# Performance work log

Measured on AMD Instinct MI355X. Metric: run time of the kernel, lower is better.

The kernel has to match this reference:

```python
import jax, jax.numpy as jnp
import numpy as np

B, N, D, H = 4, 256, 256, 8
HD = D // H
DFF = 4 * D
EPS = 1e-5


def setup_inputs() -> dict:
    key = jax.random.key(0)
    ks = jax.random.split(key, 12)
    s = 0.02
    p = lambda k, shape: (jax.random.normal(k, shape, jnp.float32) * s)
    return dict(
        h=jax.random.normal(ks[0], (B, N, D), jnp.float32),
        e=jax.random.normal(ks[1], (B, N, N, D), jnp.float32),
        We=p(ks[2], (D, D)), be=jnp.zeros((D,), jnp.float32),
        Ws=p(ks[3], (D, D)), bs=jnp.zeros((D,), jnp.float32),
        Wd=p(ks[4], (D, D)), bd=jnp.zeros((D,), jnp.float32),
        Wb=p(ks[5], (D, H)), bb=jnp.zeros((H,), jnp.float32),
        ln1_g=jnp.ones((D,), jnp.float32), ln1_b=jnp.zeros((D,), jnp.float32),
        Wqkv=p(ks[6], (D, 3 * D)), bqkv=jnp.zeros((3 * D,), jnp.float32),
        Wo=p(ks[7], (D, D)), bo=jnp.zeros((D,), jnp.float32),
        ln2_g=jnp.ones((D,), jnp.float32), ln2_b=jnp.zeros((D,), jnp.float32),
        W1=p(ks[8], (D, DFF)), b1=jnp.zeros((DFF,), jnp.float32),
        W2=p(ks[9], (DFF, D)), b2=jnp.zeros((D,), jnp.float32),
    )


def _ln(x, g, b):
    m = jnp.mean(x, axis=-1, keepdims=True)
    v = jnp.mean((x - m) ** 2, axis=-1, keepdims=True)
    return (x - m) * jax.lax.rsqrt(v + EPS) * g + b


def reference(h, e, We, be, Ws, bs, Wd, bd, Wb, bb, ln1_g, ln1_b,
              Wqkv, bqkv, Wo, bo, ln2_g, ln2_b, W1, b1, W2, b2):
    # Edge update: broadcast-add of src/dst node projections + ReLU over [B,N,N,D]
    e_new = jax.nn.relu(e @ We + be
                        + (h @ Ws + bs)[:, :, None, :]   # src -> unsqueeze(2)
                        + (h @ Wd + bd)[:, None, :, :])  # dst -> unsqueeze(1)
    # Per-head additive attention bias [B,H,N,N]
    bias = jnp.einsum('bijd,dh->bhij', e_new, Wb) + bb[None, :, None, None]
    # Pre-LN self-attention with additive bias (torch MHA, eval mode)
    x = _ln(h, ln1_g, ln1_b)
    qkv = x @ Wqkv + bqkv
    q, k, v = jnp.split(qkv, 3, axis=-1)
    q = q.reshape(B, N, H, HD)
    k = k.reshape(B, N, H, HD)
    v = v.reshape(B, N, H, HD)
    scores = jnp.einsum('bihd,bjhd->bhij', q, k) / np.float32(np.sqrt(HD)) + bias
    attn = jax.nn.softmax(scores, axis=-1)
    o = jnp.einsum('bhij,bjhd->bihd', attn, v).reshape(B, N, D)
    h1 = h + (o @ Wo + bo)
    # Pre-LN FFN (exact GELU, as torch nn.GELU default)
    y = _ln(h1, ln2_g, ln2_b)
    h2 = h1 + (jax.nn.gelu(y @ W1 + b1, approximate=False) @ W2 + b2)
    return (h2, e_new)
```

## Files before the change

kernel.cpp:

```cpp
#include <hip/hip_runtime.h>
#include <math.h>

#define EPS 1e-5f

typedef __attribute__((ext_vector_type(4))) float floatx4;
typedef __attribute__((ext_vector_type(8))) short shortx8;

__device__ __forceinline__ unsigned short f2bf(float f){
  union { float f; unsigned u; } v; v.f = f;
  unsigned r = v.u + 0x7FFFu + ((v.u >> 16) & 1u);
  return (unsigned short)(r >> 16);
}
__device__ __forceinline__ float bf2f(unsigned short s){
  union { unsigned u; float f; } v; v.u = ((unsigned)s) << 16;
  return v.f;
}

__global__ __launch_bounds__(256) void k_prep(
    const float* __restrict__ We, const float* __restrict__ Ws, const float* __restrict__ Wd,
    const float* __restrict__ Wqkv, const float* __restrict__ Wo, const float* __restrict__ W1,
    const float* __restrict__ W2, const float* __restrict__ Wb,
    unsigned short* __restrict__ WeT, unsigned short* __restrict__ WsT,
    unsigned short* __restrict__ WdT, unsigned short* __restrict__ WqkvT,
    unsigned short* __restrict__ WoT, unsigned short* __restrict__ W1T,
    unsigned short* __restrict__ W2T, unsigned short* __restrict__ WbT16)
{
  const int blk = blockIdx.x, tid = threadIdx.x;
  if (blk == 240){
#pragma unroll
    for (int hh=0; hh<8; hh++) WbT16[hh*256+tid] = f2bf(Wb[tid*8+hh]);
#pragma unroll
    for (int hh=8; hh<16; hh++) WbT16[hh*256+tid] = 0;
    return;
  }
  const float* src; unsigned short* dst; int K, N, t;
  if (blk < 16)      { src=We;   dst=WeT;   K=256;  N=256;  t=blk; }
  else if (blk < 32) { src=Ws;   dst=WsT;   K=256;  N=256;  t=blk-16; }
  else if (blk < 48) { src=Wd;   dst=WdT;   K=256;  N=256;  t=blk-32; }
  else if (blk < 96) { src=Wqkv; dst=WqkvT; K=256;  N=768;  t=blk-48; }
  else if (blk < 112){ src=Wo;   dst=WoT;   K=256;  N=256;  t=blk-96; }
  else if (blk < 176){ src=W1;   dst=W1T;   K=256;  N=1024; t=blk-112; }
  else               { src=W2;   dst=W2T;   K=1024; N=256;  t=blk-176; }
  const int tpr = N >> 6;
  const int k0 = (t / tpr) << 6, n0 = (t % tpr) << 6;
  __shared__ float tile[64][65];
#pragma unroll
  for (int s=0;s<16;s++){ int f=tid+(s<<8); int r=f>>6, c=f&63;
    tile[r][c] = src[(size_t)(k0+r)*N + n0 + c]; }
  __syncthreads();
#pragma unroll
  for (int s=0;s<16;s++){ int f=tid+(s<<8); int r=f>>6, c=f&63;
    dst[(size_t)(n0+r)*K + k0 + c] = f2bf(tile[c][r]); }
}

__global__ __launch_bounds__(256) void k_front(
  const float* __restrict__ h, const float* __restrict__ g1, const float* __restrict__ b1l,
  const float* __restrict__ bs, const float* __restrict__ be, const float* __restrict__ bd,
  const float* __restrict__ bqkv,
  const unsigned short* __restrict__ WsT, const unsigned short* __restrict__ WdT,
  const unsigned short* __restrict__ WqkvT,
  float* __restrict__ S, float* __restrict__ T,
  unsigned short* __restrict__ Qb, unsigned short* __restrict__ Kb,
  unsigned short* __restrict__ VTb)
{
  __shared__ float hs[16][256];
  __shared__ __align__(16) unsigned short xa[16*264];
  __shared__ float red1[16][16], red2[16][16];
  __shared__ float rmean[16], rinv[16];
  const int tid = threadIdx.x;
  const int rb = blockIdx.x & 63;
  const int chunk = blockIdx.x >> 6;
  const int row0 = rb * 16;
  const int b = row0 >> 8;
  const int w = tid>>6, l = tid&63, lrow = l&15, quad = l>>4;

#pragma unroll
  for (int s=0;s<4;s++){
    int f = tid + s*256; int r = f>>6, c4 = f&63;
    float4 v = ((const float4*)(h + (size_t)row0*256))[f];
    *(float4*)(&hs[r][c4*4]) = v;
  }
  __syncthreads();
  {
    int row = tid>>4, l16 = tid&15;
    if (chunk >= 2){
      float sm=0.f, sq=0.f;
#pragma unroll
      for (int j=0;j<16;j++){ float v=hs[row][l16*16+j]; sm+=v; sq+=v*v; }
      red1[row][l16]=sm; red2[row][l16]=sq;
      __syncthreads();
      if (l16==0){
        float s0=0.f,q0=0.f;
#pragma unroll
        for(int k=0;k<16;k++){ s0+=red1[row][k]; q0+=red2[row][k]; }
        float m=s0*(1.f/256.f);
        rmean[row]=m; rinv[row]=rsqrtf(q0*(1.f/256.f)-m*m+EPS);
      }
      __syncthreads();
      float m=rmean[row], iv=rinv[row];
#pragma unroll
      for (int j=0;j<16;j++){ int col=l16*16+j;
        xa[row*264+col] = f2bf((hs[row][col]-m)*iv*g1[col] + b1l[col]); }
    } else {
#pragma unroll
      for (int j=0;j<16;j++){ int col=l16*16+j; xa[row*264+col] = f2bf(hs[row][col]); }
    }
  }
  __syncthreads();
  const unsigned short* Wt;
  if (chunk==0) Wt = WsT; else if (chunk==1) Wt = WdT;
  else Wt = WqkvT + (size_t)(chunk-2)*256*256;
  floatx4 a4[4];
#pragma unroll
  for (int t=0;t<4;t++) a4[t] = (floatx4){0.f,0.f,0.f,0.f};
  for (int c=0;c<8;c++){
    shortx8 af = *(const shortx8*)(xa + lrow*264 + c*32 + quad*8);
#pragma unroll
    for (int t=0;t<4;t++){
      int n = (w*4+t)*16 + lrow;
      shortx8 bf = *(const shortx8*)(Wt + (size_t)n*256 + c*32 + quad*8);
      a4[t] = __builtin_amdgcn_mfma_f32_16x16x32_bf16(af, bf, a4[t], 0, 0, 0);
    }
  }
#pragma unroll
  for (int t=0;t<4;t++){
    int ct = w*4+t;
#pragma unroll
    for (int reg=0;reg<4;reg++){
      int row = quad*4+reg, col = ct*16+lrow;
      float v = a4[t][reg];
      if (chunk==0) S[(size_t)(row0+row)*256+col] = v + bs[col] + be[col];
      else if (chunk==1) T[(size_t)(row0+row)*256+col] = v + bd[col];
      else if (chunk==2){ float q = v + bqkv[col]; int hh=col>>5, d=col&31;
        Qb[((size_t)(b*8+hh)*256 + (row0&255)+row)*32 + d] = f2bf(q); }
      else if (chunk==3){ float q = v + bqkv[256+col]; int hh=col>>5, d=col&31;
        Kb[((size_t)(b*8+hh)*256 + (row0&255)+row)*32 + d] = f2bf(q); }
      else { float q = v + bqkv[512+col]; int hh=col>>5, d=col&31;
        VTb[((size_t)(b*8+hh)*32 + d)*256 + (row0&255)+row] = f2bf(q); }
    }
  }
}

__global__ __launch_bounds__(256, 3) void k_edge(
    const float* __restrict__ e, const unsigned short* __restrict__ WeT,
    const float* __restrict__ S, const float* __restrict__ T,
    const unsigned short* __restrict__ WbTg,
    float* __restrict__ eo, float* __restrict__ bias)
{
  __shared__ __align__(16) unsigned short En[64*264];

  const int tid = threadIdx.x;
  const int blk = blockIdx.x;
  const int jt = blk & 3;
  const int i  = (blk >> 2) & 255;
  const int b  = blk >> 10;
  const int j0 = jt * 64;
  const int w = tid >> 6, l = tid & 63;
  const int lrow = l & 15, quad = l >> 4;
  const int jloc = w*16 + lrow;

  const float* eRow = e + ((size_t)((b*256 + i)*256 + j0 + jloc)) * 256 + quad*8;
  const float* Trow = T + ((size_t)(b*256 + j0 + jloc)) * 256;
  const float* Srow = S + ((size_t)(b*256 + i)) * 256;
  const unsigned short* wBase = WeT + lrow*256 + quad*8;

  floatx4 acc[16];
#pragma unroll
  for (int t = 0; t < 16; t++) acc[t] = (floatx4){0.f,0.f,0.f,0.f};

  float4 e0 = *(const float4*)(eRow);
  float4 e1 = *(const float4*)(eRow + 4);

  for (int c = 0; c < 8; ++c){
    shortx8 ef;
    ef[0]=f2bf(e0.x); ef[1]=f2bf(e0.y); ef[2]=f2bf(e0.z); ef[3]=f2bf(e0.w);
    ef[4]=f2bf(e1.x); ef[5]=f2bf(e1.y); ef[6]=f2bf(e1.z); ef[7]=f2bf(e1.w);
    if (c < 7){
      e0 = *(const float4*)(eRow + (c+1)*32);
      e1 = *(const float4*)(eRow + (c+1)*32 + 4);
    }
    const unsigned short* wp = wBase + c*32;
#pragma unroll
    for (int t = 0; t < 16; ++t){
      shortx8 wf = *(const shortx8*)(wp + t*4096);
      acc[t] = __builtin_amdgcn_mfma_f32_16x16x32_bf16(wf, ef, acc[t], 0, 0, 0);
    }
  }

  float* eop = eo + ((size_t)((b*256 + i)*256 + j0 + jloc)) * 256;
#pragma unroll
  for (int t = 0; t < 16; ++t){
    const int d0 = t*16 + quad*4;
    float4 sv = *(const float4*)(Srow + d0);
    float4 tv = *(const float4*)(Trow + d0);
    float v0 = fmaxf(acc[t][0] + sv.x + tv.x, 0.f);
    float v1 = fmaxf(acc[t][1] + sv.y + tv.y, 0.f);
    float v2 = fmaxf(acc[t][2] + sv.z + tv.z, 0.f);
    float v3 = fmaxf(acc[t][3] + sv.w + tv.w, 0.f);
    float4 ov; ov.x = v0; ov.y = v1; ov.z = v2; ov.w = v3;
    *(float4*)(eop + d0) = ov;
    uint2 pk;
    pk.x = (unsigned int)f2bf(v0) | ((unsigned int)f2bf(v1) << 16);
    pk.y = (unsigned int)f2bf(v2) | ((unsigned int)f2bf(v3) << 16);
    *(uint2*)(En + jloc*264 + d0) = pk;
  }

  floatx4 accb = (floatx4){0.f,0.f,0.f,0.f};
#pragma unroll
  for (int c = 0; c < 8; c++){
    int k0 = c*32;
    shortx8 af = *(const shortx8*)(En + jloc*264 + k0 + quad*8);
    shortx8 bfrag = *(const shortx8*)(WbTg + lrow*256 + k0 + quad*8);
    accb = __builtin_amdgcn_mfma_f32_16x16x32_bf16(af, bfrag, accb, 0, 0, 0);
  }
  if (lrow < 8){
    float* bp = bias + ((size_t)((b*8 + lrow)*256 + i)) * 256;
    int jb = j0 + w*16 + quad*4;
#pragma unroll
    for (int r = 0; r < 4; r++) bp[jb + r] = accb[r];
  }
}

__global__ __launch_bounds__(256) void k_attn(
  const unsigned short* __restrict__ Qb, const unsigned short* __restrict__ Kb,
  const unsigned short* __restrict__ VTb, const float* __restrict__ bias,
  const float* __restrict__ bbv, unsigned short* __restrict__ Ob)
{
  __shared__ __align__(16) unsigned short Qa[32*40];
  __shared__ __align__(16) unsigned short Kl[256*40];
  __shared__ __align__(16) unsigned short Vt[32*264];
  __shared__ __align__(16) unsigned short Pl[32*264];
  __shared__ float srowm[4][16], srows[4][16], sinv[32];

  const int tid = threadIdx.x;
  const int ic = blockIdx.x & 7, bh = blockIdx.x >> 3;
  const int i0 = ic * 32;
  const int w = tid>>6, l = tid&63, lrow = l&15, quad = l>>4;

  if (tid < 128){
    int r = tid>>2, cseg = tid&3;
    *(uint4*)(Qa + r*40 + cseg*8) = ((const uint4*)(Qb + (size_t)(bh*256+i0)*32))[tid];
  }
#pragma unroll
  for (int s=0;s<4;s++){
    int f = tid + s*256; int r = f>>2, cseg = f&3;
    *(uint4*)(Kl + r*40 + cseg*8) = ((const uint4*)(Kb + (size_t)bh*8192))[f];
  }
#pragma unroll
  for (int s=0;s<4;s++){
    int f = tid + s*256; int r = f>>5, c8 = f&31;
    *(uint4*)(Vt + r*264 + c8*8) = ((const uint4*)(VTb + (size_t)bh*8192))[f];
  }
  __syncthreads();

  const int rt = w & 1, cs = (w>>1)*8;
  const float bbh = bbv[bh & 7];
  floatx4 sc[8];
  {
    shortx8 aq = *(const shortx8*)(Qa + (rt*16+lrow)*40 + quad*8);
    floatx4 z = (floatx4){0.f,0.f,0.f,0.f};
#pragma unroll
    for (int t=0;t<8;t++){
      shortx8 bk = *(const shortx8*)(Kl + ((cs+t)*16+lrow)*40 + quad*8);
      sc[t] = __builtin_amdgcn_mfma_f32_16x16x32_bf16(aq, bk, z, 0, 0, 0);
    }
  }
  const float scale = 0.17677669529663687f;
  float mx[4] = {-1e30f,-1e30f,-1e30f,-1e30f};
#pragma unroll
  for (int t=0;t<8;t++){
#pragma unroll
    for (int reg=0;reg<4;reg++){
      size_t bidx = ((size_t)(bh*256 + i0 + rt*16 + quad*4 + reg))*256 + (cs+t)*16 + lrow;
      float v = sc[t][reg]*scale + bias[bidx] + bbh;
      sc[t][reg] = v;
      mx[reg] = fmaxf(mx[reg], v);
    }
  }
#pragma unroll
  for (int m=1;m<16;m<<=1){
#pragma unroll
    for (int reg=0;reg<4;reg++) mx[reg] = fmaxf(mx[reg], __shfl_xor(mx[reg], m));
  }
  if (lrow == 0){
#pragma unroll
    for (int reg=0;reg<4;reg++) srowm[w][quad*4+reg] = mx[reg];
  }
  __syncthreads();
  float sum[4] = {0.f,0.f,0.f,0.f};
#pragma unroll
  for (int reg=0;reg<4;reg++){
    float gm = fmaxf(srowm[w][quad*4+reg], srowm[w^2][quad*4+reg]);
#pragma unroll
    for (int t=0;t<8;t++){
      float p = __expf(sc[t][reg] - gm);
      sc[t][reg] = p; sum[reg] += p;
    }
  }
#pragma unroll
  for (int m=1;m<16;m<<=1){
#pragma unroll
    for (int reg=0;reg<4;reg++) sum[reg] += __shfl_xor(sum[reg], m);
  }
  if (lrow == 0){
#pragma unroll
    for (int reg=0;reg<4;reg++) srows[w][quad*4+reg] = sum[reg];
  }
#pragma unroll
  for (int t=0;t<8;t++){
#pragma unroll
    for (int reg=0;reg<4;reg++)
      Pl[(rt*16+quad*4+reg)*264 + (cs+t)*16 + lrow] = f2bf(sc[t][reg]);
  }
  __syncthreads();
  if (lrow == 0 && w < 2){
#pragma unroll
    for (int reg=0;reg<4;reg++){
      int row = rt*16 + quad*4 + reg;
      sinv[row] = 1.f/(srows[w][quad*4+reg] + srows[w^2][quad*4+reg]);
    }
  }
  __syncthreads();
  const int rt2 = w & 1, ctd = w >> 1;
  floatx4 oc = (floatx4){0.f,0.f,0.f,0.f};
#pragma unroll
  for (int kc=0;kc<8;kc++){
    shortx8 ap = *(const shortx8*)(Pl + (rt2*16+lrow)*264 + kc*32 + quad*8);
    shortx8 bv = *(const shortx8*)(Vt + (ctd*16+lrow)*264 + kc*32 + quad*8);
    oc = __builtin_amdgcn_mfma_f32_16x16x32_bf16(ap, bv, oc, 0, 0, 0);
  }
  const int bq = bh >> 3, hh = bh & 7;
#pragma unroll
  for (int reg=0;reg<4;reg++){
    int row = rt2*16 + quad*4 + reg;
    int d = ctd*16 + lrow;
    Ob[((size_t)(bq*256 + i0 + row))*256 + hh*32 + d] = f2bf(oc[reg]*sinv[row]);
  }
}

__global__ __launch_bounds__(256) void k_back(
  const unsigned short* __restrict__ Ob, const unsigned short* __restrict__ WoT,
  const float* __restrict__ bo, const float* __restrict__ h,
  const float* __restrict__ g2, const float* __restrict__ b2l,
  const unsigned short* __restrict__ W1T, const float* __restrict__ b1f,
  const unsigned short* __restrict__ W2T, const float* __restrict__ b2f,
  float* __restrict__ out)
{
  __shared__ __align__(16) unsigned short Os[16*264];
  __shared__ float h1s[16*264];
  __shared__ __align__(16) unsigned short ys[16*264];
  __shared__ __align__(16) unsigned short Gs[16*1032];
  __shared__ float red1[16][16], red2[16][16];
  __shared__ float rmean[16], rinv[16];

  const int tid = threadIdx.x;
  const int row0 = blockIdx.x * 16;
  const int w = tid>>6, l = tid&63, lrow = l&15, quad = l>>4;

#pragma unroll
  for (int s=0;s<2;s++){
    int f = tid + s*256; int r = f>>5, c8 = f&31;
    *(uint4*)(Os + r*264 + c8*8) = ((const uint4*)(Ob + (size_t)row0*256))[f];
  }
  __syncthreads();
  {
    floatx4 a4[4];
#pragma unroll
    for (int t=0;t<4;t++) a4[t] = (floatx4){0.f,0.f,0.f,0.f};
    for (int c=0;c<8;c++){
      shortx8 af = *(const shortx8*)(Os + lrow*264 + c*32 + quad*8);
#pragma unroll
      for (int t=0;t<4;t++){
        int n = (w*4+t)*16 + lrow;
        shortx8 bf = *(const shortx8*)(WoT + (size_t)n*256 + c*32 + quad*8);
        a4[t] = __builtin_amdgcn_mfma_f32_16x16x32_bf16(af, bf, a4[t], 0, 0, 0);
      }
    }
#pragma unroll
    for (int t=0;t<4;t++){
#pragma unroll
      for (int reg=0;reg<4;reg++){
        int row = quad*4+reg, col = (w*4+t)*16+lrow;
        h1s[row*264+col] = a4[t][reg] + bo[col] + h[(size_t)(row0+row)*256 + col];
      }
    }
  }
  __syncthreads();
  {
    int row = tid>>4, l16 = tid&15;
    float sm=0.f, sq=0.f;
#pragma unroll
    for (int j=0;j<16;j++){ float v = h1s[row*264 + l16*16 + j]; sm+=v; sq+=v*v; }
    red1[row][l16]=sm; red2[row][l16]=sq;
    __syncthreads();
    if (l16==0){
      float s0=0.f,q0=0.f;
#pragma unroll
      for (int k=0;k<16;k++){ s0+=red1[row][k]; q0+=red2[row][k]; }
      float m = s0*(1.f/256.f);
      rmean[row]=m; rinv[row]=rsqrtf(q0*(1.f/256.f)-m*m+EPS);
    }
    __syncthreads();
    float m = rmean[row], iv = rinv[row];
#pragma unroll
    for (int j=0;j<16;j++){ int col = l16*16+j;
      ys[row*264+col] = f2bf((h1s[row*264+col]-m)*iv*g2[col] + b2l[col]); }
  }
  __syncthreads();
  {
    floatx4 a4[16];
#pragma unroll
    for (int t=0;t<16;t++) a4[t] = (floatx4){0.f,0.f,0.f,0.f};
    for (int c=0;c<8;c++){
      shortx8 af = *(const shortx8*)(ys + lrow*264 + c*32 + quad*8);
#pragma unroll
      for (int t=0;t<16;t++){
        int n = (w*16+t)*16 + lrow;
        shortx8 bf = *(const shortx8*)(W1T + (size_t)n*256 + c*32 + quad*8);
        a4[t] = __builtin_amdgcn_mfma_f32_16x16x32_bf16(af, bf, a4[t], 0, 0, 0);
      }
    }
#pragma unroll
    for (int t=0;t<16;t++){
#pragma unroll
      for (int reg=0;reg<4;reg++){
        int row = quad*4+reg, col = (w*16+t)*16+lrow;
        float v = a4[t][reg] + b1f[col];
        float ge = 0.5f*v*(1.f + erff(v*0.70710678118654752f));
        Gs[row*1032+col] = f2bf(ge);
      }
    }
  }
  __syncthreads();
  {
    floatx4 a4[4];
#pragma unroll
    for (int t=0;t<4;t++) a4[t] = (floatx4){0.f,0.f,0.f,0.f};
    for (int c=0;c<32;c++){
      shortx8 af = *(const shortx8*)(Gs + lrow*1032 + c*32 + quad*8);
#pragma unroll
      for (int t=0;t<4;t++){
        int n = (w*4+t)*16 + lrow;
        shortx8 bf = *(const shortx8*)(W2T + (size_t)n*1024 + c*32 + quad*8);
        a4[t] = __builtin_amdgcn_mfma_f32_16x16x32_bf16(af, bf, a4[t], 0, 0, 0);
      }
    }
#pragma unroll
    for (int t=0;t<4;t++){
#pragma unroll
      for (int reg=0;reg<4;reg++){
        int row = quad*4+reg, col = (w*4+t)*16+lrow;
        out[(size_t)(row0+row)*256+col] = h1s[row*264+col] + a4[t][reg] + b2f[col];
      }
    }
  }
}

extern "C" void kernel_launch(void* const* d_in, const int* in_sizes, int n_in,
                              void* d_out, int out_size, void* d_ws, size_t ws_size,
                              hipStream_t stream)
{
  (void)in_sizes; (void)n_in; (void)out_size; (void)ws_size;
  const float* h    = (const float*)d_in[0];
  const float* e    = (const float*)d_in[1];
  const float* We   = (const float*)d_in[2];
  const float* be   = (const float*)d_in[3];
  const float* Ws   = (const float*)d_in[4];
  const float* bs   = (const float*)d_in[5];
  const float* Wd   = (const float*)d_in[6];
  const float* bd   = (const float*)d_in[7];
  const float* Wb   = (const float*)d_in[8];
  const float* bb   = (const float*)d_in[9];
  const float* g1   = (const float*)d_in[10];
  const float* b1l  = (const float*)d_in[11];
  const float* Wqkv = (const float*)d_in[12];
  const float* bqkv = (const float*)d_in[13];
  const float* Wo   = (const float*)d_in[14];
  const float* bo   = (const float*)d_in[15];
  const float* g2   = (const float*)d_in[16];
  const float* b2l  = (const float*)d_in[17];
  const float* W1   = (const float*)d_in[18];
  const float* b1f  = (const float*)d_in[19];
  const float* W2   = (const float*)d_in[20];
  const float* b2f  = (const float*)d_in[21];

  float* out  = (float*)d_out;
  float* h2_o = out;
  float* e_o  = out + 262144;

  float* wsf = (float*)d_ws;
  unsigned short* ush = (unsigned short*)d_ws;
  unsigned short* WeT   = ush;
  unsigned short* WsT   = ush + 65536;
  unsigned short* WdT   = ush + 131072;
  unsigned short* WqkvT = ush + 196608;
  unsigned short* WoT   = ush + 393216;
  unsigned short* W1T   = ush + 458752;
  unsigned short* W2T   = ush + 720896;
  unsigned short* WbT16 = ush + 983040;
  float* S_   = wsf + 493568;
  float* T_   = wsf + 755712;
  float* bias = wsf + 1017856;
  unsigned short* Qb  = (unsigned short*)(wsf + 3115008);
  unsigned short* Kb  = (unsigned short*)(wsf + 3246080);
  unsigned short* VTb = (unsigned short*)(wsf + 3377152);
  unsigned short* Ob  = (unsigned short*)(wsf + 3508224);

  k_prep <<<dim3(241),  dim3(256), 0, stream>>>(We,Ws,Wd,Wqkv,Wo,W1,W2,Wb,
                                                WeT,WsT,WdT,WqkvT,WoT,W1T,W2T,WbT16);
  k_front<<<dim3(320),  dim3(256), 0, stream>>>(h, g1,b1l, bs,be,bd, bqkv,
                                                WsT,WdT,WqkvT, S_,T_, Qb,Kb,VTb);
  k_edge <<<dim3(4096), dim3(256), 0, stream>>>(e, WeT, S_, T_, WbT16, e_o, bias);
  k_attn <<<dim3(256),  dim3(256), 0, stream>>>(Qb, Kb, VTb, bias, bb, Ob);
  k_back <<<dim3(64),   dim3(256), 0, stream>>>(Ob, WoT, bo, h, g2,b2l,
                                                W1T,b1f, W2T,b2f, h2_o);
}
```

Before: 783.4 us.

## Stage edge GEMM tiles in LDS with register-prefetched K-chunks

Reworks the edge-update GEMM in k_edge. It now cooperatively loads 64-wide K chunks of e (converted to bf16) and of the WeT weights into padded shared memory, with the next chunk prefetched into registers while MFMAs run on the current one. Each wave now computes a 64x64 output tile and reuses weight fragments across four j-groups, replacing the old scheme where every wave read all of WeT from global memory. The src projection row is cached in shared memory. The cost is more LDS use (about 46 KB), which may reduce occupancy under the 3-blocks launch bound, and extra barriers.

```diff
diff --git a/kernel.cpp b/kernel.cpp
--- a/kernel.cpp
+++ b/kernel.cpp
@@ -147,7 +147,11 @@
     const unsigned short* __restrict__ WbTg,
     float* __restrict__ eo, float* __restrict__ bias)
 {
-  __shared__ __align__(16) unsigned short En[64*264];
+  __shared__ __align__(16) unsigned short smem[23040];
+  __shared__ float sbuf[256];
+  unsigned short* As = smem;
+  unsigned short* Bs = smem + 4608;
+  unsigned short* En = smem;
 
   const int tid = threadIdx.x;
   const int blk = blockIdx.x;
@@ -157,59 +161,106 @@
   const int j0 = jt * 64;
   const int w = tid >> 6, l = tid & 63;
   const int lrow = l & 15, quad = l >> 4;
-  const int jloc = w*16 + lrow;
-
-  const float* eRow = e + ((size_t)((b*256 + i)*256 + j0 + jloc)) * 256 + quad*8;
-  const float* Trow = T + ((size_t)(b*256 + j0 + jloc)) * 256;
-  const float* Srow = S + ((size_t)(b*256 + i)) * 256;
-  const unsigned short* wBase = WeT + lrow*256 + quad*8;
-
-  floatx4 acc[16];
-#pragma unroll
-  for (int t = 0; t < 16; t++) acc[t] = (floatx4){0.f,0.f,0.f,0.f};
-
-  float4 e0 = *(const float4*)(eRow);
-  float4 e1 = *(const float4*)(eRow + 4);
-
-  for (int c = 0; c < 8; ++c){
-    shortx8 ef;
-    ef[0]=f2bf(e0.x); ef[1]=f2bf(e0.y); ef[2]=f2bf(e0.z); ef[3]=f2bf(e0.w);
-    ef[4]=f2bf(e1.x); ef[5]=f2bf(e1.y); ef[6]=f2bf(e1.z); ef[7]=f2bf(e1.w);
-    if (c < 7){
-      e0 = *(const float4*)(eRow + (c+1)*32);
-      e1 = *(const float4*)(eRow + (c+1)*32 + 4);
-    }
-    const unsigned short* wp = wBase + c*32;
-#pragma unroll
-    for (int t = 0; t < 16; ++t){
-      shortx8 wf = *(const shortx8*)(wp + t*4096);
-      acc[t] = __builtin_amdgcn_mfma_f32_16x16x32_bf16(wf, ef, acc[t], 0, 0, 0);
-    }
-  }
-
-  float* eop = eo + ((size_t)((b*256 + i)*256 + j0 + jloc)) * 256;
-#pragma unroll
-  for (int t = 0; t < 16; ++t){
-    const int d0 = t*16 + quad*4;
-    float4 sv = *(const float4*)(Srow + d0);
-    float4 tv = *(const float4*)(Trow + d0);
-    float v0 = fmaxf(acc[t][0] + sv.x + tv.x, 0.f);
-    float v1 = fmaxf(acc[t][1] + sv.y + tv.y, 0.f);
-    float v2 = fmaxf(acc[t][2] + sv.z + tv.z, 0.f);
-    float v3 = fmaxf(acc[t][3] + sv.w + tv.w, 0.f);
-    float4 ov; ov.x = v0; ov.y = v1; ov.z = v2; ov.w = v3;
-    *(float4*)(eop + d0) = ov;
+
+  sbuf[tid] = S[((b << 8) + i) * 256 + tid];
+
+  const float* eBase = e + ((size_t)((b*256 + i)*256 + j0)) * 256;
+  const int rE = tid >> 4;
+  const int cE = (tid & 15) * 4;
+  const int nW = tid >> 3;
+  const int sW = (tid & 7) * 8;
+
+  float4 pe[4]; uint4 pw[8];
+#pragma unroll
+  for (int s=0;s<4;s++) pe[s] = *(const float4*)(eBase + (size_t)(rE + s*16)*256 + cE);
+#pragma unroll
+  for (int s=0;s<8;s++) pw[s] = *(const uint4*)(WeT + (size_t)(nW + s*32)*256 + sW);
+#pragma unroll
+  for (int s=0;s<4;s++){
     uint2 pk;
-    pk.x = (unsigned int)f2bf(v0) | ((unsigned int)f2bf(v1) << 16);
-    pk.y = (unsigned int)f2bf(v2) | ((unsigned int)f2bf(v3) << 16);
-    *(uint2*)(En + jloc*264 + d0) = pk;
-  }
+    pk.x = (unsigned)f2bf(pe[s].x) | ((unsigned)f2bf(pe[s].y) << 16);
+    pk.y = (unsigned)f2bf(pe[s].z) | ((unsigned)f2bf(pe[s].w) << 16);
+    *(uint2*)(As + (rE + s*16)*72 + cE) = pk;
+  }
+#pragma unroll
+  for (int s=0;s<8;s++) *(uint4*)(Bs + (nW + s*32)*72 + sW) = pw[s];
+  __syncthreads();
+
+  floatx4 acc[4][4];
+#pragma unroll
+  for (int jg=0;jg<4;jg++)
+#pragma unroll
+    for (int t=0;t<4;t++) acc[jg][t] = (floatx4){0.f,0.f,0.f,0.f};
+
+  for (int c = 0; c < 4; ++c){
+    if (c < 3){
+      const int k0 = (c+1)*64;
+#pragma unroll
+      for (int s=0;s<4;s++) pe[s] = *(const float4*)(eBase + (size_t)(rE + s*16)*256 + k0 + cE);
+#pragma unroll
+      for (int s=0;s<8;s++) pw[s] = *(const uint4*)(WeT + (size_t)(nW + s*32)*256 + k0 + sW);
+    }
+#pragma unroll
+    for (int ks=0;ks<2;ks++){
+      shortx8 ef0 = *(const shortx8*)(As + ( 0 + lrow)*72 + ks*32 + quad*8);
+      shortx8 ef1 = *(const shortx8*)(As + (16 + lrow)*72 + ks*32 + quad*8);
+      shortx8 ef2 = *(const shortx8*)(As + (32 + lrow)*72 + ks*32 + quad*8);
+      shortx8 ef3 = *(const shortx8*)(As + (48 + lrow)*72 + ks*32 + quad*8);
+#pragma unroll
+      for (int t=0;t<4;t++){
+        shortx8 wf = *(const shortx8*)(Bs + ((w*4+t)*16 + lrow)*72 + ks*32 + quad*8);
+        acc[0][t] = __builtin_amdgcn_mfma_f32_16x16x32_bf16(wf, ef0, acc[0][t], 0, 0, 0);
+        acc[1][t] = __builtin_amdgcn_mfma_f32_16x16x32_bf16(wf, ef1, acc[1][t], 0, 0, 0);
+        acc[2][t] = __builtin_amdgcn_mfma_f32_16x16x32_bf16(wf, ef2, acc[2][t], 0, 0, 0);
+        acc[3][t] = __builtin_amdgcn_mfma_f32_16x16x32_bf16(wf, ef3, acc[3][t], 0, 0, 0);
+      }
+    }
+    __syncthreads();
+    if (c < 3){
+#pragma unroll
+      for (int s=0;s<4;s++){
+        uint2 pk;
+        pk.x = (unsigned)f2bf(pe[s].x) | ((unsigned)f2bf(pe[s].y) << 16);
+        pk.y = (unsigned)f2bf(pe[s].z) | ((unsigned)f2bf(pe[s].w) << 16);
+        *(uint2*)(As + (rE + s*16)*72 + cE) = pk;
+      }
+#pragma unroll
+      for (int s=0;s<8;s++) *(uint4*)(Bs + (nW + s*32)*72 + sW) = pw[s];
+      __syncthreads();
+    }
+  }
+
+  const float* Tb = T + (size_t)(b*256 + j0) * 256;
+  float* eop = eo + ((size_t)((b*256 + i)*256 + j0)) * 256;
+#pragma unroll
+  for (int jg=0;jg<4;jg++){
+    const int jl = jg*16 + lrow;
+    const float* Trow = Tb + (size_t)jl*256;
+    float* erow = eop + (size_t)jl*256;
+#pragma unroll
+    for (int t=0;t<4;t++){
+      const int d0 = (w*4+t)*16 + quad*4;
+      float4 sv = *(const float4*)(&sbuf[d0]);
+      float4 tv = *(const float4*)(Trow + d0);
+      float v0 = fmaxf(acc[jg][t][0] + sv.x + tv.x, 0.f);
+      float v1 = fmaxf(acc[jg][t][1] + sv.y + tv.y, 0.f);
+      float v2 = fmaxf(acc[jg][t][2] + sv.z + tv.z, 0.f);
+      float v3 = fmaxf(acc[jg][t][3] + sv.w + tv.w, 0.f);
+      float4 ov; ov.x = v0; ov.y = v1; ov.z = v2; ov.w = v3;
+      *(float4*)(erow + d0) = ov;
+      uint2 pk;
+      pk.x = (unsigned)f2bf(v0) | ((unsigned)f2bf(v1) << 16);
+      pk.y = (unsigned)f2bf(v2) | ((unsigned)f2bf(v3) << 16);
+      *(uint2*)(En + jl*264 + d0) = pk;
+    }
+  }
+  __syncthreads();
 
   floatx4 accb = (floatx4){0.f,0.f,0.f,0.f};
 #pragma unroll
-  for (int c = 0; c < 8; c++){
-    int k0 = c*32;
-    shortx8 af = *(const shortx8*)(En + jloc*264 + k0 + quad*8);
+  for (int c8 = 0; c8 < 8; c8++){
+    int k0 = c8*32;
+    shortx8 af = *(const shortx8*)(En + (w*16 + lrow)*264 + k0 + quad*8);
     shortx8 bfrag = *(const shortx8*)(WbTg + lrow*256 + k0 + quad*8);
     accb = __builtin_amdgcn_mfma_f32_16x16x32_bf16(af, bfrag, accb, 0, 0, 0);
   }
```

After: 735.5 us. 6.1% less time.
